# Kernel optimization log

Measured on AMD Instinct MI355X. Metric: run time of the kernel, lower is better.

The kernel has to match this reference:

```python
import jax, jax.numpy as jnp
import numpy as np


def gcn_conv(x, W, src, dst, edge_weight, n_nodes):
    """PyG GCNConv (bias=False, add_self_loops=True, normalize=True).
    out = D^{-1/2} (A + I) D^{-1/2} X W, with deg computed from edge weights
    into each destination node plus the self-loop weight 1.
    """
    h = x @ W  # [N, F_out]
    deg = jax.ops.segment_sum(edge_weight, dst, num_segments=n_nodes) + 1.0  # self-loop w=1
    dinv = jax.lax.rsqrt(deg)  # deg >= 1 so safe
    norm = dinv[src] * edge_weight * dinv[dst]  # [E]
    # gather -> weight -> scatter-add
    agg = jax.ops.segment_sum(norm[:, None] * h[src], dst, num_segments=n_nodes)
    # self-loop contribution: norm_ii = deg_i^{-1}
    return agg + h * (1.0 / deg)[:, None]


def setup_inputs() -> dict:
    key = jax.random.key(0)
    k1, k2, k3, k4, k5 = jax.random.split(key, 5)
    N, E = 10000, 160000
    in_ch, hidden, out_ch = 512, 512, 256
    x = jax.random.normal(k1, (N, in_ch), dtype=jnp.float32)
    edge_index = jax.random.randint(k2, (2, E), 0, N, dtype=jnp.int64)
    edge_weight = jax.random.uniform(k3, (E,), dtype=jnp.float32)
    # Glorot-style init like torch_geometric.nn.dense.linear
    W1 = jax.random.normal(k4, (in_ch, hidden), dtype=jnp.float32) * (1.0 / np.sqrt(in_ch))
    W2 = jax.random.normal(k5, (hidden, out_ch), dtype=jnp.float32) * (1.0 / np.sqrt(hidden))
    return {"x": x, "edge_index": edge_index, "edge_weight": edge_weight, "W1": W1, "W2": W2}


def reference(x, edge_index, edge_weight, W1, W2):
    n_nodes = x.shape[0]
    src, dst = edge_index[0], edge_index[1]
    h = jax.nn.relu(gcn_conv(x, W1, src, dst, edge_weight, n_nodes))
    # dropout is identity in eval mode
    return gcn_conv(h, W2, src, dst, edge_weight, n_nodes)
```

## Files before the change

kernel.cpp:

```cpp
#include <hip/hip_runtime.h>

#define N_NODES 10000
#define N_EDGES 160000
#define M_PAD   10112
#define MT      79
#define KT      8
#define ELLW    64

typedef short s8v __attribute__((ext_vector_type(8)));
typedef short s4v __attribute__((ext_vector_type(4)));
typedef float f4v __attribute__((ext_vector_type(4)));

__device__ inline short f2bf(float f) {
    unsigned u = __builtin_bit_cast(unsigned, f);
    u += 0x7FFF + ((u >> 16) & 1);
    return (short)(u >> 16);
}
__device__ inline float bf2f(short s) {
    return __builtin_bit_cast(float, ((unsigned)(unsigned short)s) << 16);
}

#define GLD_LDS16(g, l)                                                      \
    __builtin_amdgcn_global_load_lds(                                        \
        (const __attribute__((address_space(1))) unsigned int*)(g),          \
        (__attribute__((address_space(3))) unsigned int*)(l), 16, 0, 0)

__global__ __launch_bounds__(256) void k_prep(const float* __restrict__ W1,
                                              const float* __restrict__ W2,
                                              char* __restrict__ w1T,
                                              char* __restrict__ w2T,
                                              float* __restrict__ deg,
                                              int* __restrict__ count) {
    int bid = blockIdx.x;
    if (bid < 192) {
        const float* W;
        char* out;
        int ncols, t;
        if (bid < 128) { W = W1; out = w1T; ncols = 512; t = bid * 256 + threadIdx.x; }
        else           { W = W2; out = w2T; ncols = 256; t = (bid - 128) * 256 + threadIdx.x; }
        int n = t >> 6;
        int c = t & 63;
        s8v v;
#pragma unroll
        for (int j = 0; j < 8; j++) v[j] = f2bf(W[(long long)(c * 8 + j) * ncols + n]);
        int r = n & 127, tn = n >> 7, tk = c >> 3, sc = c & 7;
        int slot = sc ^ (r & 7);
        *(s8v*)&out[(((long long)tn * KT + tk) << 14) + r * 128 + slot * 16] = v;
    } else {
        int i = (bid - 192) * 256 + threadIdx.x;
        if (i < N_NODES) { deg[i] = 1.0f; count[i] = 0; }
    }
}

__device__ __forceinline__ void xcd_map(int b, int& by, int& bx) {
    by = (b & 7) * 10 + ((b >> 3) >> 2);
    bx = (b >> 3) & 3;
}

__global__ __launch_bounds__(256) void k_gemm1_deg(const float* __restrict__ x,
                                                   const char* __restrict__ w1T,
                                                   short* __restrict__ Cb,
                                                   const int* __restrict__ src,
                                                   const int* __restrict__ dst,
                                                   const float* __restrict__ wgt,
                                                   float* __restrict__ deg,
                                                   int* __restrict__ count,
                                                   int2* __restrict__ ell) {
    int bid = blockIdx.x;
    if (bid >= 320) {
        int e = (bid - 320) * 256 + threadIdx.x;
        if (e < N_EDGES) {
            int d = dst[e];
            float wv = wgt[e];
            atomicAdd(&deg[d], wv);
            int pos = atomicAdd(&count[d], 1);
            if (pos < ELLW)
                ell[(long long)d * ELLW + pos] = make_int2(src[e], __float_as_int(wv));
        }
        return;
    }
    int by, bx;
    xcd_map(bid, by, bx);
    if (by >= MT) return;

    __shared__ char As[16384];
    __shared__ char Bs[16384];
    int tid = threadIdx.x, lane = tid & 63, w = tid >> 6;
    int wr = w >> 1, wc = w & 1;

    const char* gb = w1T + ((long long)bx * KT << 14);

    f4v acc[4][4];
#pragma unroll
    for (int m = 0; m < 4; m++)
#pragma unroll
        for (int n = 0; n < 4; n++) acc[m][n] = (f4v){0.f, 0.f, 0.f, 0.f};

    for (int kt = 0; kt < KT; ++kt) {
#pragma unroll
        for (int it = 0; it < 8; ++it) {
            int c = it * 256 + tid;
            int r = c >> 4, f4 = c & 15;
            int gr = by * 128 + r;
            float4 v = make_float4(0.f, 0.f, 0.f, 0.f);
            if (gr < N_NODES) v = *(const float4*)&x[(long long)gr * 512 + kt * 64 + f4 * 4];
            s4v b;
            b[0] = f2bf(v.x); b[1] = f2bf(v.y); b[2] = f2bf(v.z); b[3] = f2bf(v.w);
            int slot = (f4 >> 1) ^ (r & 7);
            *(s4v*)&As[r * 128 + slot * 16 + (f4 & 1) * 8] = b;
        }
        const char* b0 = gb + (kt << 14);
#pragma unroll
        for (int j = 0; j < 4; ++j) {
            int off = (j * 256 + w * 64) * 16;
            GLD_LDS16(b0 + off + lane * 16, Bs + off);
        }
        __syncthreads();

#pragma unroll
        for (int kk = 0; kk < 2; ++kk) {
            s8v a[4], b[4];
#pragma unroll
            for (int m = 0; m < 4; ++m) {
                int r = wr * 64 + m * 16 + (lane & 15);
                int slot = ((lane >> 4) + kk * 4) ^ (r & 7);
                a[m] = *(const s8v*)&As[r * 128 + slot * 16];
            }
#pragma unroll
            for (int n = 0; n < 4; ++n) {
                int r = wc * 64 + n * 16 + (lane & 15);
                int slot = ((lane >> 4) + kk * 4) ^ (r & 7);
                b[n] = *(const s8v*)&Bs[r * 128 + slot * 16];
            }
#pragma unroll
            for (int m = 0; m < 4; ++m)
#pragma unroll
                for (int n = 0; n < 4; ++n)
                    acc[m][n] = __builtin_amdgcn_mfma_f32_16x16x32_bf16(a[m], b[n], acc[m][n], 0, 0, 0);
        }
        __syncthreads();
    }

    int row0 = by * 128 + wr * 64;
    int col0 = bx * 128 + wc * 64;
#pragma unroll
    for (int m = 0; m < 4; ++m) {
#pragma unroll
        for (int q = 0; q < 4; ++q) {
            int row = row0 + m * 16 + (lane >> 4) * 4 + q;
            if (row < N_NODES) {
#pragma unroll
                for (int n = 0; n < 4; ++n) {
                    int col = col0 + n * 16 + (lane & 15);
                    Cb[(long long)row * 512 + col] = f2bf(acc[m][n][q]);
                }
            }
        }
    }
}

__global__ __launch_bounds__(256) void k_gemm2(const char* __restrict__ A,
                                               const char* __restrict__ w2T,
                                               short* __restrict__ Cb) {
    int by, bx;
    xcd_map(blockIdx.x, by, bx);
    if (by >= MT) return;

    __shared__ char As[16384];
    __shared__ char Bs[8192];
    int tid = threadIdx.x, lane = tid & 63, w = tid >> 6;
    int wr = w >> 1, wc = w & 1;

    const char* ga = A + ((long long)by * KT << 14);
    const char* gbase = w2T + ((long long)(bx >> 1) * KT << 14) + (bx & 1) * 8192;

    f4v acc[4][2];
#pragma unroll
    for (int m = 0; m < 4; m++)
#pragma unroll
        for (int n = 0; n < 2; n++) acc[m][n] = (f4v){0.f, 0.f, 0.f, 0.f};

    for (int kt = 0; kt < KT; ++kt) {
        const char* a0 = ga + (kt << 14);
        const char* b0 = gbase + (kt << 14);
#pragma unroll
        for (int j = 0; j < 4; ++j) {
            int off = (j * 256 + w * 64) * 16;
            GLD_LDS16(a0 + off + lane * 16, As + off);
        }
#pragma unroll
        for (int j = 0; j < 2; ++j) {
            int off = (j * 256 + w * 64) * 16;
            GLD_LDS16(b0 + off + lane * 16, Bs + off);
        }
        __syncthreads();

#pragma unroll
        for (int kk = 0; kk < 2; ++kk) {
            s8v a[4], b[2];
#pragma unroll
            for (int m = 0; m < 4; ++m) {
                int r = wr * 64 + m * 16 + (lane & 15);
                int slot = ((lane >> 4) + kk * 4) ^ (r & 7);
                a[m] = *(const s8v*)&As[r * 128 + slot * 16];
            }
#pragma unroll
            for (int n = 0; n < 2; ++n) {
                int r = wc * 32 + n * 16 + (lane & 15);
                int slot = ((lane >> 4) + kk * 4) ^ (r & 7);
                b[n] = *(const s8v*)&Bs[r * 128 + slot * 16];
            }
#pragma unroll
            for (int m = 0; m < 4; ++m)
#pragma unroll
                for (int n = 0; n < 2; ++n)
                    acc[m][n] = __builtin_amdgcn_mfma_f32_16x16x32_bf16(a[m], b[n], acc[m][n], 0, 0, 0);
        }
        __syncthreads();
    }

    int row0 = by * 128 + wr * 64;
    int col0 = bx * 64 + wc * 32;
#pragma unroll
    for (int m = 0; m < 4; ++m) {
#pragma unroll
        for (int q = 0; q < 4; ++q) {
            int row = row0 + m * 16 + (lane >> 4) * 4 + q;
            if (row < N_NODES) {
#pragma unroll
                for (int n = 0; n < 2; ++n) {
                    int col = col0 + n * 16 + (lane & 15);
                    Cb[(long long)row * 256 + col] = f2bf(acc[m][n][q]);
                }
            }
        }
    }
}

template <int F, bool RELU, bool OUT_TILED>
__global__ __launch_bounds__(256) void k_gather(const int2* __restrict__ ell,
                                                const int* __restrict__ count,
                                                const short* __restrict__ hb,
                                                const float* __restrict__ deg,
                                                void* __restrict__ outp,
                                                int n_waves) {
    const int FPT = F / 64;
    int wave = (int)((blockIdx.x * (long long)blockDim.x + threadIdx.x) >> 6);
    if (wave >= n_waves) return;
    int lane = threadIdx.x & 63;

    float acc[FPT];
#pragma unroll
    for (int j = 0; j < FPT; j++) acc[j] = 0.f;

    if (wave < N_NODES) {
        float dg = deg[wave];
        float inv = 1.0f / dg;
        float dinv_d = rsqrtf(dg);
        {
            if constexpr (FPT == 8) {
                s8v v = *(const s8v*)&hb[(long long)wave * F + lane * 8];
#pragma unroll
                for (int j = 0; j < 8; j++) acc[j] = bf2f(v[j]) * inv;
            } else {
                s4v v = *(const s4v*)&hb[(long long)wave * F + lane * 4];
#pragma unroll
                for (int j = 0; j < 4; j++) acc[j] = bf2f(v[j]) * inv;
            }
        }
        int cnt = count[wave];
        if (cnt > ELLW) cnt = ELLW;
        const int2* row = &ell[(long long)wave * ELLW];
        int p = 0;
        for (; p + 3 < cnt; p += 4) {
            int2 e0 = row[p], e1 = row[p + 1], e2 = row[p + 2], e3 = row[p + 3];
            float n0 = rsqrtf(deg[e0.x]) * __int_as_float(e0.y) * dinv_d;
            float n1 = rsqrtf(deg[e1.x]) * __int_as_float(e1.y) * dinv_d;
            float n2 = rsqrtf(deg[e2.x]) * __int_as_float(e2.y) * dinv_d;
            float n3 = rsqrtf(deg[e3.x]) * __int_as_float(e3.y) * dinv_d;
            if constexpr (FPT == 8) {
                s8v v0 = *(const s8v*)&hb[(long long)e0.x * F + lane * 8];
                s8v v1 = *(const s8v*)&hb[(long long)e1.x * F + lane * 8];
                s8v v2 = *(const s8v*)&hb[(long long)e2.x * F + lane * 8];
                s8v v3 = *(const s8v*)&hb[(long long)e3.x * F + lane * 8];
#pragma unroll
                for (int j = 0; j < 8; j++)
                    acc[j] += n0 * bf2f(v0[j]) + n1 * bf2f(v1[j]) + n2 * bf2f(v2[j]) + n3 * bf2f(v3[j]);
            } else {
                s4v v0 = *(const s4v*)&hb[(long long)e0.x * F + lane * 4];
                s4v v1 = *(const s4v*)&hb[(long long)e1.x * F + lane * 4];
                s4v v2 = *(const s4v*)&hb[(long long)e2.x * F + lane * 4];
                s4v v3 = *(const s4v*)&hb[(long long)e3.x * F + lane * 4];
#pragma unroll
                for (int j = 0; j < 4; j++)
                    acc[j] += n0 * bf2f(v0[j]) + n1 * bf2f(v1[j]) + n2 * bf2f(v2[j]) + n3 * bf2f(v3[j]);
            }
        }
        for (; p < cnt; ++p) {
            int2 e0 = row[p];
            float n0 = rsqrtf(deg[e0.x]) * __int_as_float(e0.y) * dinv_d;
            if constexpr (FPT == 8) {
                s8v v0 = *(const s8v*)&hb[(long long)e0.x * F + lane * 8];
#pragma unroll
                for (int j = 0; j < 8; j++) acc[j] += n0 * bf2f(v0[j]);
            } else {
                s4v v0 = *(const s4v*)&hb[(long long)e0.x * F + lane * 4];
#pragma unroll
                for (int j = 0; j < 4; j++) acc[j] += n0 * bf2f(v0[j]);
            }
        }
        if (RELU) {
#pragma unroll
            for (int j = 0; j < FPT; j++) acc[j] = fmaxf(acc[j], 0.f);
        }
    }

    if constexpr (OUT_TILED) {
        s8v v;
#pragma unroll
        for (int j = 0; j < 8; j++) v[j] = f2bf(acc[j]);
        int tm = wave >> 7, r = wave & 127, tk = lane >> 3, sc = lane & 7;
        int slot = sc ^ (r & 7);
        char* out = (char*)outp;
        *(s8v*)&out[(((long long)tm * KT + tk) << 14) + r * 128 + slot * 16] = v;
    } else {
        float* out = (float*)outp + (long long)wave * F + lane * FPT;
#pragma unroll
        for (int j = 0; j < FPT; j += 4) {
            *(float4*)&out[j] = make_float4(acc[j], acc[j + 1], acc[j + 2], acc[j + 3]);
        }
    }
}

extern "C" void kernel_launch(void* const* d_in, const int* in_sizes, int n_in,
                              void* d_out, int out_size, void* d_ws, size_t ws_size,
                              hipStream_t stream) {
    const float* x  = (const float*)d_in[0];
    const int*   ei = (const int*)d_in[1];
    const float* w  = (const float*)d_in[2];
    const float* W1 = (const float*)d_in[3];
    const float* W2 = (const float*)d_in[4];
    float* out = (float*)d_out;

    const int* src = ei;
    const int* dst = ei + N_EDGES;

    char* p = (char*)d_ws;
    auto alloc = [&](size_t bytes) {
        char* r = p;
        p += (bytes + 255) & ~(size_t)255;
        return r;
    };
    char*  a1_bf  = alloc((size_t)MT * KT * 16384);
    char*  w1T    = alloc((size_t)4 * KT * 16384);
    char*  w2T    = alloc((size_t)2 * KT * 16384);
    short* h1_bf  = (short*)alloc((size_t)N_NODES * 512 * 2);
    short* h2_bf  = (short*)alloc((size_t)N_NODES * 256 * 2);
    float* deg    = (float*)alloc(N_NODES * 4);
    int*   count  = (int*)alloc(N_NODES * 4);
    int2*  ell    = (int2*)alloc((size_t)N_NODES * ELLW * 8);

    const int B = 256;

    k_prep<<<232, B, 0, stream>>>(W1, W2, w1T, w2T, deg, count);
    k_gemm1_deg<<<320 + 625, B, 0, stream>>>(x, w1T, h1_bf, src, dst, w, deg, count, ell);
    k_gather<512, true, true><<<(M_PAD * 64) / B, B, 0, stream>>>(
        ell, count, h1_bf, deg, a1_bf, M_PAD);
    k_gemm2<<<320, B, 0, stream>>>(a1_bf, w2T, h2_bf);
    k_gather<256, false, false><<<(N_NODES * 64) / B, B, 0, stream>>>(
        ell, count, h2_bf, deg, out, N_NODES);
}
```

Baseline: 102.0 us.

## Pre-convert x to tiled bf16 in prep kernel; unroll gather by eight

After: 88.31 us. -13.4%, faster.

```diff
diff --git a/kernel.cpp b/kernel.cpp
--- a/kernel.cpp
+++ b/kernel.cpp
@@ -25,19 +25,37 @@
         (const __attribute__((address_space(1))) unsigned int*)(g),          \
         (__attribute__((address_space(3))) unsigned int*)(l), 16, 0, 0)
 
-__global__ __launch_bounds__(256) void k_prep(const float* __restrict__ W1,
+__global__ __launch_bounds__(256) void k_prep(const float* __restrict__ x,
+                                              const float* __restrict__ W1,
                                               const float* __restrict__ W2,
+                                              char* __restrict__ x_bf,
                                               char* __restrict__ w1T,
                                               char* __restrict__ w2T,
                                               float* __restrict__ deg,
                                               int* __restrict__ count) {
     int bid = blockIdx.x;
-    if (bid < 192) {
+    if (bid < 2528) {
+        long long t = (long long)bid * 256 + threadIdx.x;
+        int gr = (int)(t >> 6);
+        int c  = (int)(t & 63);
+        s8v v;
+        if (gr < N_NODES) {
+            const float* p = &x[(long long)gr * 512 + c * 8];
+#pragma unroll
+            for (int j = 0; j < 8; j++) v[j] = f2bf(p[j]);
+        } else {
+#pragma unroll
+            for (int j = 0; j < 8; j++) v[j] = 0;
+        }
+        int r = gr & 127, tm = gr >> 7, tk = c >> 3, sc = c & 7;
+        int slot = sc ^ (r & 7);
+        *(s8v*)&x_bf[(((long long)tm * KT + tk) << 14) + r * 128 + slot * 16] = v;
+    } else if (bid < 2720) {
         const float* W;
         char* out;
         int ncols, t;
-        if (bid < 128) { W = W1; out = w1T; ncols = 512; t = bid * 256 + threadIdx.x; }
-        else           { W = W2; out = w2T; ncols = 256; t = (bid - 128) * 256 + threadIdx.x; }
+        if (bid < 2656) { W = W1; out = w1T; ncols = 512; t = (bid - 2528) * 256 + threadIdx.x; }
+        else            { W = W2; out = w2T; ncols = 256; t = (bid - 2656) * 256 + threadIdx.x; }
         int n = t >> 6;
         int c = t & 63;
         s8v v;
@@ -47,18 +65,80 @@
         int slot = sc ^ (r & 7);
         *(s8v*)&out[(((long long)tn * KT + tk) << 14) + r * 128 + slot * 16] = v;
     } else {
-        int i = (bid - 192) * 256 + threadIdx.x;
+        int i = (bid - 2720) * 256 + threadIdx.x;
         if (i < N_NODES) { deg[i] = 1.0f; count[i] = 0; }
     }
 }
 
-__device__ __forceinline__ void xcd_map(int b, int& by, int& bx) {
-    by = (b & 7) * 10 + ((b >> 3) >> 2);
-    bx = (b >> 3) & 3;
-}
-
-__global__ __launch_bounds__(256) void k_gemm1_deg(const float* __restrict__ x,
-                                                   const char* __restrict__ w1T,
+__device__ __forceinline__ void gemm_block(const char* __restrict__ ga,
+                                           const char* __restrict__ gb,
+                                           short* __restrict__ Cb,
+                                           int M, int N, int row_blk, int col_blk,
+                                           char* As, char* Bs) {
+    int tid = threadIdx.x, lane = tid & 63, w = tid >> 6;
+    int wr = w >> 1, wc = w & 1;
+
+    f4v acc[4][4];
+#pragma unroll
+    for (int m = 0; m < 4; m++)
+#pragma unroll
+        for (int n = 0; n < 4; n++) acc[m][n] = (f4v){0.f, 0.f, 0.f, 0.f};
+
+    for (int kt = 0; kt < KT; ++kt) {
+        const char* a0 = ga + (kt << 14);
+        const char* b0 = gb + (kt << 14);
+#pragma unroll
+        for (int j = 0; j < 4; ++j) {
+            int off = (j * 256 + w * 64) * 16;
+            GLD_LDS16(a0 + off + lane * 16, As + off);
+            GLD_LDS16(b0 + off + lane * 16, Bs + off);
+        }
+        __syncthreads();
+
+#pragma unroll
+        for (int kk = 0; kk < 2; ++kk) {
+            s8v a[4], b[4];
+#pragma unroll
+            for (int m = 0; m < 4; ++m) {
+                int r = wr * 64 + m * 16 + (lane & 15);
+                int slot = ((lane >> 4) + kk * 4) ^ (r & 7);
+                a[m] = *(const s8v*)&As[r * 128 + slot * 16];
+            }
+#pragma unroll
+            for (int n = 0; n < 4; ++n) {
+                int r = wc * 64 + n * 16 + (lane & 15);
+                int slot = ((lane >> 4) + kk * 4) ^ (r & 7);
+                b[n] = *(const s8v*)&Bs[r * 128 + slot * 16];
+            }
+#pragma unroll
+            for (int m = 0; m < 4; ++m)
+#pragma unroll
+                for (int n = 0; n < 4; ++n)
+                    acc[m][n] = __builtin_amdgcn_mfma_f32_16x16x32_bf16(a[m], b[n], acc[m][n], 0, 0, 0);
+        }
+        __syncthreads();
+    }
+
+    int row0 = row_blk * 128 + wr * 64;
+    int col0 = col_blk * 128 + wc * 64;
+#pragma unroll
+    for (int m = 0; m < 4; ++m) {
+#pragma unroll
+        for (int q = 0; q < 4; ++q) {
+            int row = row0 + m * 16 + (lane >> 4) * 4 + q;
+            if (row < M) {
+#pragma unroll
+                for (int n = 0; n < 4; ++n) {
+                    int col = col0 + n * 16 + (lane & 15);
+                    Cb[(long long)row * N + col] = f2bf(acc[m][n][q]);
+                }
+            }
+        }
+    }
+}
+
+__global__ __launch_bounds__(256) void k_gemm1_deg(const char* __restrict__ A,
+                                                   const char* __restrict__ B,
                                                    short* __restrict__ Cb,
                                                    const int* __restrict__ src,
                                                    const int* __restrict__ dst,
@@ -67,8 +147,8 @@
                                                    int* __restrict__ count,
                                                    int2* __restrict__ ell) {
     int bid = blockIdx.x;
-    if (bid >= 320) {
-        int e = (bid - 320) * 256 + threadIdx.x;
+    if (bid >= 316) {
+        int e = (bid - 316) * 256 + threadIdx.x;
         if (e < N_EDGES) {
             int d = dst[e];
             float wv = wgt[e];
@@ -79,84 +159,16 @@
         }
         return;
     }
-    int by, bx;
-    xcd_map(bid, by, bx);
-    if (by >= MT) return;
-
     __shared__ char As[16384];
     __shared__ char Bs[16384];
-    int tid = threadIdx.x, lane = tid & 63, w = tid >> 6;
-    int wr = w >> 1, wc = w & 1;
-
-    const char* gb = w1T + ((long long)bx * KT << 14);
-
-    f4v acc[4][4];
-#pragma unroll
-    for (int m = 0; m < 4; m++)
-#pragma unroll
-        for (int n = 0; n < 4; n++) acc[m][n] = (f4v){0.f, 0.f, 0.f, 0.f};
-
-    for (int kt = 0; kt < KT; ++kt) {
-#pragma unroll
-        for (int it = 0; it < 8; ++it) {
-            int c = it * 256 + tid;
-            int r = c >> 4, f4 = c & 15;
-            int gr = by * 128 + r;
-            float4 v = make_float4(0.f, 0.f, 0.f, 0.f);
-            if (gr < N_NODES) v = *(const float4*)&x[(long long)gr * 512 + kt * 64 + f4 * 4];
-            s4v b;
-            b[0] = f2bf(v.x); b[1] = f2bf(v.y); b[2] = f2bf(v.z); b[3] = f2bf(v.w);
-            int slot = (f4 >> 1) ^ (r & 7);
-            *(s4v*)&As[r * 128 + slot * 16 + (f4 & 1) * 8] = b;
-        }
-        const char* b0 = gb + (kt << 14);
-#pragma unroll
-        for (int j = 0; j < 4; ++j) {
-            int off = (j * 256 + w * 64) * 16;
-            GLD_LDS16(b0 + off + lane * 16, Bs + off);
-        }
-        __syncthreads();
-
-#pragma unroll
-        for (int kk = 0; kk < 2; ++kk) {
-            s8v a[4], b[4];
-#pragma unroll
-            for (int m = 0; m < 4; ++m) {
-                int r = wr * 64 + m * 16 + (lane & 15);
-                int slot = ((lane >> 4) + kk * 4) ^ (r & 7);
-                a[m] = *(const s8v*)&As[r * 128 + slot * 16];
-            }
-#pragma unroll
-            for (int n = 0; n < 4; ++n) {
-                int r = wc * 64 + n * 16 + (lane & 15);
-                int slot = ((lane >> 4) + kk * 4) ^ (r & 7);
-                b[n] = *(const s8v*)&Bs[r * 128 + slot * 16];
-            }
-#pragma unroll
-            for (int m = 0; m < 4; ++m)
-#pragma unroll
-                for (int n = 0; n < 4; ++n)
-                    acc[m][n] = __builtin_amdgcn_mfma_f32_16x16x32_bf16(a[m], b[n], acc[m][n], 0, 0, 0);
-        }
-        __syncthreads();
-    }
-
-    int row0 = by * 128 + wr * 64;
-    int col0 = bx * 128 + wc * 64;
-#pragma unroll
-    for (int m = 0; m < 4; ++m) {
-#pragma unroll
-        for (int q = 0; q < 4; ++q) {
-            int row = row0 + m * 16 + (lane >> 4) * 4 + q;
-            if (row < N_NODES) {
-#pragma unroll
-                for (int n = 0; n < 4; ++n) {
-                    int col = col0 + n * 16 + (lane & 15);
-                    Cb[(long long)row * 512 + col] = f2bf(acc[m][n][q]);
-                }
-            }
-        }
-    }
+    int bx = bid & 3, by = bid >> 2;
+    gemm_block(A + ((long long)by * KT << 14), B + ((long long)bx * KT << 14),
+               Cb, N_NODES, 512, by, bx, As, Bs);
+}
+
+__device__ __forceinline__ void xcd_map(int b, int& by, int& bx) {
+    by = (b & 7) * 10 + ((b >> 3) >> 2);
+    bx = (b >> 3) & 3;
 }
 
 __global__ __launch_bounds__(256) void k_gemm2(const char* __restrict__ A,
@@ -272,6 +284,36 @@
         if (cnt > ELLW) cnt = ELLW;
         const int2* row = &ell[(long long)wave * ELLW];
         int p = 0;
+        for (; p + 7 < cnt; p += 8) {
+            int2 e[8];
+#pragma unroll
+            for (int q = 0; q < 8; q++) e[q] = row[p + q];
+            float nn[8];
+#pragma unroll
+            for (int q = 0; q < 8; q++)
+                nn[q] = rsqrtf(deg[e[q].x]) * __int_as_float(e[q].y) * dinv_d;
+            if constexpr (FPT == 8) {
+                s8v v[8];
+#pragma unroll
+                for (int q = 0; q < 8; q++)
+                    v[q] = *(const s8v*)&hb[(long long)e[q].x * F + lane * 8];
+#pragma unroll
+                for (int j = 0; j < 8; j++) {
+#pragma unroll
+                    for (int q = 0; q < 8; q++) acc[j] += nn[q] * bf2f(v[q][j]);
+                }
+            } else {
+                s4v v[8];
+#pragma unroll
+                for (int q = 0; q < 8; q++)
+                    v[q] = *(const s4v*)&hb[(long long)e[q].x * F + lane * 4];
+#pragma unroll
+                for (int j = 0; j < 4; j++) {
+#pragma unroll
+                    for (int q = 0; q < 8; q++) acc[j] += nn[q] * bf2f(v[q][j]);
+                }
+            }
+        }
         for (; p + 3 < cnt; p += 4) {
             int2 e0 = row[p], e1 = row[p + 1], e2 = row[p + 2], e3 = row[p + 3];
             float n0 = rsqrtf(deg[e0.x]) * __int_as_float(e0.y) * dinv_d;
@@ -351,6 +393,7 @@
         p += (bytes + 255) & ~(size_t)255;
         return r;
     };
+    char*  x_bf   = alloc((size_t)MT * KT * 16384);
     char*  a1_bf  = alloc((size_t)MT * KT * 16384);
     char*  w1T    = alloc((size_t)4 * KT * 16384);
     char*  w2T    = alloc((size_t)2 * KT * 16384);
@@ -362,8 +405,8 @@
 
     const int B = 256;
 
-    k_prep<<<232, B, 0, stream>>>(W1, W2, w1T, w2T, deg, count);
-    k_gemm1_deg<<<320 + 625, B, 0, stream>>>(x, w1T, h1_bf, src, dst, w, deg, count, ell);
+    k_prep<<<2760, B, 0, stream>>>(x, W1, W2, x_bf, w1T, w2T, deg, count);
+    k_gemm1_deg<<<316 + 625, B, 0, stream>>>(x_bf, w1T, h1_bf, src, dst, w, deg, count, ell);
     k_gather<512, true, true><<<(M_PAD * 64) / B, B, 0, stream>>>(
         ell, count, h1_bf, deg, a1_bf, M_PAD);
     k_gemm2<<<320, B, 0, stream>>>(a1_bf, w2T, h2_bf);
```
